# Performance work log

Hardware: AMD Instinct MI355X
Metric: run time of the kernel (lower is better)

## Reference

```python
import jax, jax.numpy as jnp
import numpy as np

B, F, C, T, K, S = 2048, 4096, 8192, 8, 1024, 8

def setup_inputs() -> dict:
    key = jax.random.key(0)
    k1, k2, k3, k4 = jax.random.split(key, 4)
    x = jax.random.uniform(k1, (B, F), dtype=jnp.float32)  # soft truth values in [0,1]
    conj_feat = jax.random.randint(k2, (C, T), 0, F, dtype=jnp.int32)   # feature index per literal
    conj_sign = jax.random.randint(k3, (C, T), 0, 2, dtype=jnp.int32)   # 1 -> positive literal, 0 -> negated
    class_conj = jax.random.randint(k4, (K, S), 0, C, dtype=jnp.int32)  # conjunct ids feeding each class OR
    return {"x": x, "conj_feat": conj_feat, "conj_sign": conj_sign, "class_conj": class_conj}

def reference(x, conj_feat, conj_sign, class_conj):
    # AND layer: gather literals and take product over each conjunct's terms.
    lits = x[:, conj_feat]                       # [B, C, T] gather
    lits = jnp.where(conj_sign > 0, lits, 1.0 - lits)
    conj_vals = jnp.prod(lits, axis=-1)          # [B, C]  fuzzy AND
    # OR layer: per-class max over its member conjuncts.
    disj_vals = jnp.max(conj_vals[:, class_conj], axis=-1)  # [B, K]
    return disj_vals
```

## Files before the change

kernel.cpp:

```cpp
#include <hip/hip_runtime.h>
#include <hip/hip_fp16.h>

#define B_ 2048
#define F_ 4096
#define C_ 8192
#define T_ 8
#define K_ 1024
#define S_ 8
#define RROWS 8
#define TPB 1024

__global__ void build_klit_kernel(const int* __restrict__ feat,
                                  const int* __restrict__ sign,
                                  const int* __restrict__ class_conj,
                                  uint4* __restrict__ klit) {
    int j = blockIdx.x * blockDim.x + threadIdx.x;
    if (j >= K_ * S_) return;
    int k = j & (K_ - 1);
    int s = j >> 10;
    int c = class_conj[k * S_ + s];
    const int* fr = feat + c * T_;
    const int* sr = sign + c * T_;
    unsigned t[T_];
    #pragma unroll
    for (int i = 0; i < T_; ++i)
        t[i] = (unsigned)((fr[i] << 1) | (sr[i] > 0 ? 1 : 0)) & 0xFFFFu;
    uint4 p;
    p.x = t[0] | (t[1] << 16);
    p.y = t[2] | (t[3] << 16);
    p.z = t[4] | (t[5] << 16);
    p.w = t[6] | (t[7] << 16);
    klit[j] = p;
}

__device__ __forceinline__ __half2 h2max(__half2 a, __half2 b) {
    unsigned int ua = *(unsigned int*)&a, ub = *(unsigned int*)&b, ur;
    asm("v_pk_max_f16 %0, %1, %2" : "=v"(ur) : "v"(ua), "v"(ub));
    return *(__half2*)&ur;
}

__device__ __forceinline__ __half2 u2h2(unsigned int u) { return *(__half2*)&u; }

#define LIT_INIT(SLOT)                                              \
    { uint4 g = xs4[SLOT];                                          \
      pa = u2h2(g.x); pb = u2h2(g.y); pc = u2h2(g.z); pd = u2h2(g.w); }
#define LIT_MUL(SLOT)                                               \
    { uint4 g = xs4[SLOT];                                          \
      pa = __hmul2(pa, u2h2(g.x)); pb = __hmul2(pb, u2h2(g.y));     \
      pc = __hmul2(pc, u2h2(g.z)); pd = __hmul2(pd, u2h2(g.w)); }

__global__ __launch_bounds__(TPB, 4) void dnf_kernel(
    const float* __restrict__ x,
    const uint4* __restrict__ klit,
    float* __restrict__ out)
{
    __shared__ __align__(16) uint4 xs4[F_ * 2];

    const int b0  = blockIdx.x * RROWS;
    const int tid = threadIdx.x;

    for (int f = tid; f < F_; f += TPB) {
        float v0 = x[(size_t)(b0 + 0) * F_ + f];
        float v1 = x[(size_t)(b0 + 1) * F_ + f];
        float v2 = x[(size_t)(b0 + 2) * F_ + f];
        float v3 = x[(size_t)(b0 + 3) * F_ + f];
        float v4 = x[(size_t)(b0 + 4) * F_ + f];
        float v5 = x[(size_t)(b0 + 5) * F_ + f];
        float v6 = x[(size_t)(b0 + 6) * F_ + f];
        float v7 = x[(size_t)(b0 + 7) * F_ + f];
        __half2 n01 = __floats2half2_rn(1.0f - v0, 1.0f - v1);
        __half2 n23 = __floats2half2_rn(1.0f - v2, 1.0f - v3);
        __half2 n45 = __floats2half2_rn(1.0f - v4, 1.0f - v5);
        __half2 n67 = __floats2half2_rn(1.0f - v6, 1.0f - v7);
        __half2 p01 = __floats2half2_rn(v0, v1);
        __half2 p23 = __floats2half2_rn(v2, v3);
        __half2 p45 = __floats2half2_rn(v4, v5);
        __half2 p67 = __floats2half2_rn(v6, v7);
        uint4 neg, pos;
        neg.x = *(unsigned*)&n01; neg.y = *(unsigned*)&n23;
        neg.z = *(unsigned*)&n45; neg.w = *(unsigned*)&n67;
        pos.x = *(unsigned*)&p01; pos.y = *(unsigned*)&p23;
        pos.z = *(unsigned*)&p45; pos.w = *(unsigned*)&p67;
        xs4[(f << 1) | 0] = neg;
        xs4[(f << 1) | 1] = pos;
    }
    __syncthreads();

    const int kk = tid;

    __half2 ma, mb, mc, md;
    #pragma unroll
    for (int s = 0; s < S_; ++s) {
        uint4 p = klit[s * K_ + kk];
        __half2 pa, pb, pc, pd;
        LIT_INIT(p.x & 0xFFFFu);
        LIT_MUL (p.x >> 16);
        LIT_MUL (p.y & 0xFFFFu);
        LIT_MUL (p.y >> 16);
        LIT_MUL (p.z & 0xFFFFu);
        LIT_MUL (p.z >> 16);
        LIT_MUL (p.w & 0xFFFFu);
        LIT_MUL (p.w >> 16);
        if (s == 0) { ma = pa; mb = pb; mc = pc; md = pd; }
        else {
            ma = h2max(ma, pa); mb = h2max(mb, pb);
            mc = h2max(mc, pc); md = h2max(md, pd);
        }
    }

    float2 f;
    f = __half22float2(ma); out[(size_t)(b0+0)*K_+kk] = f.x; out[(size_t)(b0+1)*K_+kk] = f.y;
    f = __half22float2(mb); out[(size_t)(b0+2)*K_+kk] = f.x; out[(size_t)(b0+3)*K_+kk] = f.y;
    f = __half22float2(mc); out[(size_t)(b0+4)*K_+kk] = f.x; out[(size_t)(b0+5)*K_+kk] = f.y;
    f = __half22float2(md); out[(size_t)(b0+6)*K_+kk] = f.x; out[(size_t)(b0+7)*K_+kk] = f.y;
}

__global__ __launch_bounds__(TPB, 4) void dnf_kernel_nows(
    const float* __restrict__ x,
    const int* __restrict__ feat,
    const int* __restrict__ sign,
    const int* __restrict__ class_conj,
    float* __restrict__ out)
{
    __shared__ __align__(16) uint4 xs4[F_ * 2];

    const int b0  = blockIdx.x * RROWS;
    const int tid = threadIdx.x;

    for (int f = tid; f < F_; f += TPB) {
        float v0 = x[(size_t)(b0 + 0) * F_ + f];
        float v1 = x[(size_t)(b0 + 1) * F_ + f];
        float v2 = x[(size_t)(b0 + 2) * F_ + f];
        float v3 = x[(size_t)(b0 + 3) * F_ + f];
        float v4 = x[(size_t)(b0 + 4) * F_ + f];
        float v5 = x[(size_t)(b0 + 5) * F_ + f];
        float v6 = x[(size_t)(b0 + 6) * F_ + f];
        float v7 = x[(size_t)(b0 + 7) * F_ + f];
        __half2 n01 = __floats2half2_rn(1.0f - v0, 1.0f - v1);
        __half2 n23 = __floats2half2_rn(1.0f - v2, 1.0f - v3);
        __half2 n45 = __floats2half2_rn(1.0f - v4, 1.0f - v5);
        __half2 n67 = __floats2half2_rn(1.0f - v6, 1.0f - v7);
        __half2 p01 = __floats2half2_rn(v0, v1);
        __half2 p23 = __floats2half2_rn(v2, v3);
        __half2 p45 = __floats2half2_rn(v4, v5);
        __half2 p67 = __floats2half2_rn(v6, v7);
        uint4 neg, pos;
        neg.x = *(unsigned*)&n01; neg.y = *(unsigned*)&n23;
        neg.z = *(unsigned*)&n45; neg.w = *(unsigned*)&n67;
        pos.x = *(unsigned*)&p01; pos.y = *(unsigned*)&p23;
        pos.z = *(unsigned*)&p45; pos.w = *(unsigned*)&p67;
        xs4[(f << 1) | 0] = neg;
        xs4[(f << 1) | 1] = pos;
    }
    __syncthreads();

    const int kk = tid;
    const int4* cc = (const int4*)(class_conj + kk * S_);
    int4 a0 = cc[0], a1 = cc[1];
    int idx[S_] = {a0.x, a0.y, a0.z, a0.w, a1.x, a1.y, a1.z, a1.w};

    __half2 ma, mb, mc, md;
    #pragma unroll
    for (int s = 0; s < S_; ++s) {
        int c = idx[s];
        const int4* fq = (const int4*)(feat + c * T_);
        const int4* sq = (const int4*)(sign + c * T_);
        int4 f0 = fq[0], f1 = fq[1];
        int4 s0 = sq[0], s1 = sq[1];
        __half2 pa, pb, pc, pd;
        unsigned o;
        o = (f0.x << 1) | (s0.x > 0 ? 1 : 0); LIT_INIT(o);
        o = (f0.y << 1) | (s0.y > 0 ? 1 : 0); LIT_MUL(o);
        o = (f0.z << 1) | (s0.z > 0 ? 1 : 0); LIT_MUL(o);
        o = (f0.w << 1) | (s0.w > 0 ? 1 : 0); LIT_MUL(o);
        o = (f1.x << 1) | (s1.x > 0 ? 1 : 0); LIT_MUL(o);
        o = (f1.y << 1) | (s1.y > 0 ? 1 : 0); LIT_MUL(o);
        o = (f1.z << 1) | (s1.z > 0 ? 1 : 0); LIT_MUL(o);
        o = (f1.w << 1) | (s1.w > 0 ? 1 : 0); LIT_MUL(o);
        if (s == 0) { ma = pa; mb = pb; mc = pc; md = pd; }
        else {
            ma = h2max(ma, pa); mb = h2max(mb, pb);
            mc = h2max(mc, pc); md = h2max(md, pd);
        }
    }

    float2 f;
    f = __half22float2(ma); out[(size_t)(b0+0)*K_+kk] = f.x; out[(size_t)(b0+1)*K_+kk] = f.y;
    f = __half22float2(mb); out[(size_t)(b0+2)*K_+kk] = f.x; out[(size_t)(b0+3)*K_+kk] = f.y;
    f = __half22float2(mc); out[(size_t)(b0+4)*K_+kk] = f.x; out[(size_t)(b0+5)*K_+kk] = f.y;
    f = __half22float2(md); out[(size_t)(b0+6)*K_+kk] = f.x; out[(size_t)(b0+7)*K_+kk] = f.y;
}

extern "C" void kernel_launch(void* const* d_in, const int* in_sizes, int n_in,
                              void* d_out, int out_size, void* d_ws, size_t ws_size,
                              hipStream_t stream) {
    const float* x  = (const float*)d_in[0];
    const int* feat = (const int*)d_in[1];
    const int* sign = (const int*)d_in[2];
    const int* ccj  = (const int*)d_in[3];
    float* out      = (float*)d_out;

    const size_t klit_bytes = (size_t)K_ * S_ * sizeof(uint4);
    if (ws_size >= klit_bytes) {
        uint4* klit = (uint4*)d_ws;
        build_klit_kernel<<<(K_ * S_ + 255) / 256, 256, 0, stream>>>(feat, sign, ccj, klit);
        dnf_kernel<<<B_ / RROWS, TPB, 0, stream>>>(x, klit, out);
    } else {
        dnf_kernel_nows<<<B_ / RROWS, TPB, 0, stream>>>(x, feat, sign, ccj, out);
    }
}
```

Measured before the change: 21.46 us.

## Reorder literal gathers to balance LDS banks and prefetch klit before staging

The literal-index builder now greedily reorders each conjunct's eight literals so that, at each product step, the lanes of a wavefront spread their shared-memory gathers across bank groups rather than colliding. The point is to cut LDS bank conflicts in the main gather-multiply loop; because multiplication commutes, the results stay the same. The main kernel also loads all eight klit entries into registers before the x staging loop, which overlaps that global latency with staging at the cost of extra registers. The builder kernel becomes much heavier, with many barriers and shared atomics per block, and its run time counts toward the total.

```diff
diff --git a/kernel.cpp b/kernel.cpp
--- a/kernel.cpp
+++ b/kernel.cpp
@@ -10,27 +10,65 @@
 #define RROWS 8
 #define TPB 1024
 
-__global__ void build_klit_kernel(const int* __restrict__ feat,
-                                  const int* __restrict__ sign,
-                                  const int* __restrict__ class_conj,
-                                  uint4* __restrict__ klit) {
-    int j = blockIdx.x * blockDim.x + threadIdx.x;
-    if (j >= K_ * S_) return;
-    int k = j & (K_ - 1);
-    int s = j >> 10;
-    int c = class_conj[k * S_ + s];
-    const int* fr = feat + c * T_;
-    const int* sr = sign + c * T_;
-    unsigned t[T_];
-    #pragma unroll
-    for (int i = 0; i < T_; ++i)
-        t[i] = (unsigned)((fr[i] << 1) | (sr[i] > 0 ? 1 : 0)) & 0xFFFFu;
+__global__ __launch_bounds__(64) void build_klit_balanced(
+    const int* __restrict__ feat,
+    const int* __restrict__ sign,
+    const int* __restrict__ class_conj,
+    uint4* __restrict__ klit)
+{
+    const int s    = blockIdx.x & 7;
+    const int wgrp = blockIdx.x >> 3;
+    const int tid  = threadIdx.x;
+    const int kk   = wgrp * 64 + tid;
+
+    const int c = class_conj[kk * S_ + s];
+    const int4* fq = (const int4*)(feat + c * T_);
+    const int4* sq = (const int4*)(sign + c * T_);
+    int4 f0 = fq[0], f1 = fq[1];
+    int4 s0 = sq[0], s1 = sq[1];
+    unsigned slots[T_];
+    slots[0] = (unsigned)((f0.x << 1) | (s0.x > 0 ? 1 : 0));
+    slots[1] = (unsigned)((f0.y << 1) | (s0.y > 0 ? 1 : 0));
+    slots[2] = (unsigned)((f0.z << 1) | (s0.z > 0 ? 1 : 0));
+    slots[3] = (unsigned)((f0.w << 1) | (s0.w > 0 ? 1 : 0));
+    slots[4] = (unsigned)((f1.x << 1) | (s1.x > 0 ? 1 : 0));
+    slots[5] = (unsigned)((f1.y << 1) | (s1.y > 0 ? 1 : 0));
+    slots[6] = (unsigned)((f1.z << 1) | (s1.z > 0 ? 1 : 0));
+    slots[7] = (unsigned)((f1.w << 1) | (s1.w > 0 ? 1 : 0));
+
+    __shared__ int cnt[8];
+    unsigned used = 0;
+    unsigned chosen[T_];
+
+    for (int j = 0; j < T_; ++j) {
+        if (tid < 8) cnt[tid] = 0;
+        __syncthreads();
+        for (int r = 0; r < 8; ++r) {
+            if ((tid & 7) == r) {
+                int best = -1, bc = 1 << 30;
+                const int rot = tid >> 3;
+                #pragma unroll
+                for (int ii = 0; ii < T_; ++ii) {
+                    int i = (ii + rot) & 7;
+                    if (!((used >> i) & 1u)) {
+                        int cg = cnt[slots[i] & 7];
+                        if (cg < bc) { bc = cg; best = i; }
+                    }
+                }
+                used |= 1u << best;
+                chosen[j] = slots[best];
+                atomicAdd(&cnt[(int)(slots[best] & 7)], 1);
+            }
+            __syncthreads();
+        }
+    }
+
     uint4 p;
-    p.x = t[0] | (t[1] << 16);
-    p.y = t[2] | (t[3] << 16);
-    p.z = t[4] | (t[5] << 16);
-    p.w = t[6] | (t[7] << 16);
-    klit[j] = p;
+    p.x = (chosen[0] & 0xFFFFu) | (chosen[1] << 16);
+    p.y = (chosen[2] & 0xFFFFu) | (chosen[3] << 16);
+    p.z = (chosen[4] & 0xFFFFu) | (chosen[5] << 16);
+    p.w = (chosen[6] & 0xFFFFu) | (chosen[7] << 16);
+    klit[s * K_ + kk] = p;
 }
 
 __device__ __forceinline__ __half2 h2max(__half2 a, __half2 b) {
@@ -49,6 +87,22 @@
       pa = __hmul2(pa, u2h2(g.x)); pb = __hmul2(pb, u2h2(g.y));     \
       pc = __hmul2(pc, u2h2(g.z)); pd = __hmul2(pd, u2h2(g.w)); }
 
+#define STEP_FIRST(P)                                               \
+    { __half2 pa, pb, pc, pd;                                       \
+      LIT_INIT((P).x & 0xFFFFu); LIT_MUL((P).x >> 16);              \
+      LIT_MUL ((P).y & 0xFFFFu); LIT_MUL((P).y >> 16);              \
+      LIT_MUL ((P).z & 0xFFFFu); LIT_MUL((P).z >> 16);              \
+      LIT_MUL ((P).w & 0xFFFFu); LIT_MUL((P).w >> 16);              \
+      ma = pa; mb = pb; mc = pc; md = pd; }
+#define STEP_NEXT(P)                                                \
+    { __half2 pa, pb, pc, pd;                                       \
+      LIT_INIT((P).x & 0xFFFFu); LIT_MUL((P).x >> 16);              \
+      LIT_MUL ((P).y & 0xFFFFu); LIT_MUL((P).y >> 16);              \
+      LIT_MUL ((P).z & 0xFFFFu); LIT_MUL((P).z >> 16);              \
+      LIT_MUL ((P).w & 0xFFFFu); LIT_MUL((P).w >> 16);              \
+      ma = h2max(ma, pa); mb = h2max(mb, pb);                       \
+      mc = h2max(mc, pc); md = h2max(md, pd); }
+
 __global__ __launch_bounds__(TPB, 4) void dnf_kernel(
     const float* __restrict__ x,
     const uint4* __restrict__ klit,
@@ -58,6 +112,16 @@
 
     const int b0  = blockIdx.x * RROWS;
     const int tid = threadIdx.x;
+    const int kk  = tid;
+
+    uint4 kl0 = klit[0 * K_ + kk];
+    uint4 kl1 = klit[1 * K_ + kk];
+    uint4 kl2 = klit[2 * K_ + kk];
+    uint4 kl3 = klit[3 * K_ + kk];
+    uint4 kl4 = klit[4 * K_ + kk];
+    uint4 kl5 = klit[5 * K_ + kk];
+    uint4 kl6 = klit[6 * K_ + kk];
+    uint4 kl7 = klit[7 * K_ + kk];
 
     for (int f = tid; f < F_; f += TPB) {
         float v0 = x[(size_t)(b0 + 0) * F_ + f];
@@ -86,27 +150,15 @@
     }
     __syncthreads();
 
-    const int kk = tid;
-
     __half2 ma, mb, mc, md;
-    #pragma unroll
-    for (int s = 0; s < S_; ++s) {
-        uint4 p = klit[s * K_ + kk];
-        __half2 pa, pb, pc, pd;
-        LIT_INIT(p.x & 0xFFFFu);
-        LIT_MUL (p.x >> 16);
-        LIT_MUL (p.y & 0xFFFFu);
-        LIT_MUL (p.y >> 16);
-        LIT_MUL (p.z & 0xFFFFu);
-        LIT_MUL (p.z >> 16);
-        LIT_MUL (p.w & 0xFFFFu);
-        LIT_MUL (p.w >> 16);
-        if (s == 0) { ma = pa; mb = pb; mc = pc; md = pd; }
-        else {
-            ma = h2max(ma, pa); mb = h2max(mb, pb);
-            mc = h2max(mc, pc); md = h2max(md, pd);
-        }
-    }
+    STEP_FIRST(kl0);
+    STEP_NEXT(kl1);
+    STEP_NEXT(kl2);
+    STEP_NEXT(kl3);
+    STEP_NEXT(kl4);
+    STEP_NEXT(kl5);
+    STEP_NEXT(kl6);
+    STEP_NEXT(kl7);
 
     float2 f;
     f = __half22float2(ma); out[(size_t)(b0+0)*K_+kk] = f.x; out[(size_t)(b0+1)*K_+kk] = f.y;
@@ -203,7 +255,7 @@
     const size_t klit_bytes = (size_t)K_ * S_ * sizeof(uint4);
     if (ws_size >= klit_bytes) {
         uint4* klit = (uint4*)d_ws;
-        build_klit_kernel<<<(K_ * S_ + 255) / 256, 256, 0, stream>>>(feat, sign, ccj, klit);
+        build_klit_balanced<<<K_ * S_ / 64, 64, 0, stream>>>(feat, sign, ccj, klit);
         dnf_kernel<<<B_ / RROWS, TPB, 0, stream>>>(x, klit, out);
     } else {
         dnf_kernel_nows<<<B_ / RROWS, TPB, 0, stream>>>(x, feat, sign, ccj, out);
```

Result: slower. 54.11 us (+152.2%).
